# Kernel tuning notes

Hardware: AMD Instinct MI355X
Metric: run time of the kernel (lower is better)

Reference implementation:

```python
import jax, jax.numpy as jnp
import numpy as np

GROUPS = 32
EPS = 1e-5   # nn.GroupNorm default


def group_norm(x, gamma, beta):
    # x: [B, C, H, W]
    b, c, h, w = x.shape
    xg = x.reshape(b, GROUPS, c // GROUPS, h, w)
    mu = jnp.mean(xg, axis=(2, 3, 4), keepdims=True)
    var = jnp.var(xg, axis=(2, 3, 4), keepdims=True)
    xn = ((xg - mu) * jax.lax.rsqrt(var + EPS)).reshape(b, c, h, w)
    return xn * gamma[None, :, None, None] + beta[None, :, None, None]


def conv1x1(x, w, b):
    # x: [B, C, H, W], w: [O, C], b: [O]
    return jnp.einsum('bchw,oc->bohw', x, w) + b[None, :, None, None]


def setup_inputs() -> dict:
    key = jax.random.key(0)
    ks = jax.random.split(key, 10)
    B, C, H, W = 8, 512, 64, 64
    std = 1.0 / np.sqrt(C)
    inp = {
        'x': jax.random.normal(ks[0], (B, C, H, W), dtype=jnp.float32),
        'gn_gamma': jnp.ones((C,), dtype=jnp.float32),
        'gn_beta': jnp.zeros((C,), dtype=jnp.float32),
        'wq': jax.random.normal(ks[1], (C, C), dtype=jnp.float32) * std,
        'bq': jnp.zeros((C,), dtype=jnp.float32),
        'wk': jax.random.normal(ks[2], (C, C), dtype=jnp.float32) * std,
        'bk': jnp.zeros((C,), dtype=jnp.float32),
        'wv': jax.random.normal(ks[3], (C, C), dtype=jnp.float32) * std,
        'bv': jnp.zeros((C,), dtype=jnp.float32),
        'wp': jax.random.normal(ks[4], (C, C), dtype=jnp.float32) * std,
        'bp': jnp.zeros((C,), dtype=jnp.float32),
    }
    return inp


def reference(x, gn_gamma, gn_beta, wq, bq, wk, bk, wv, bv, wp, bp):
    b, c, hh, ww = x.shape
    n = hh * ww
    h = group_norm(x, gn_gamma, gn_beta)
    q = conv1x1(h, wq, bq).reshape(b, c, n).transpose(0, 2, 1)  # [B, N, C]
    k = conv1x1(h, wk, bk).reshape(b, c, n)                     # [B, C, N]
    v = conv1x1(h, wv, bv).reshape(b, c, n).transpose(0, 2, 1)  # [B, N, C]
    scale = 1.0 / jnp.sqrt(jnp.asarray(c, dtype=x.dtype))
    attn = jax.nn.softmax(jnp.einsum('bnc,bcm->bnm', q, k) * scale, axis=-1)
    out = jnp.einsum('bnm,bmc->bnc', attn, v)                   # [B, N, C]
    out = out.transpose(0, 2, 1).reshape(b, c, hh, ww)
    return x + conv1x1(out, wp, bp)
```

## Files before the change

kernel.cpp:

```cpp
#include <hip/hip_runtime.h>


typedef __attribute__((ext_vector_type(8))) __bf16 bf16x8;
typedef __attribute__((ext_vector_type(4))) float f32x4;
typedef unsigned int u32;

#define DEVICE __device__ __forceinline__

DEVICE void async_copy16(const void* g, void* l) {
  __builtin_amdgcn_global_load_lds(
      (__attribute__((address_space(1))) u32*)(g),
      (__attribute__((address_space(3))) u32*)(l),
      16, 0, 0);
}

__global__ __launch_bounds__(256) void cvt_w(
    const float* __restrict__ w0, const float* __restrict__ w1,
    const float* __restrict__ w2, const float* __restrict__ w3,
    __bf16* __restrict__ o0, __bf16* __restrict__ o1,
    __bf16* __restrict__ o2, __bf16* __restrict__ o3) {
  int idx = blockIdx.x * 256 + threadIdx.x;
  int off = idx * 8;
  int m = off >> 18;
  int r = off & 262143;
  const float* src = m == 0 ? w0 : m == 1 ? w1 : m == 2 ? w2 : w3;
  __bf16* dst = m == 0 ? o0 : m == 1 ? o1 : m == 2 ? o2 : o3;
  float4 a = *(const float4*)(src + r);
  float4 b = *(const float4*)(src + r + 4);
  bf16x8 v = {(__bf16)a.x, (__bf16)a.y, (__bf16)a.z, (__bf16)a.w,
              (__bf16)b.x, (__bf16)b.y, (__bf16)b.z, (__bf16)b.w};
  *(bf16x8*)(dst + r) = v;
}

__global__ __launch_bounds__(256) void gn_stats(const float* __restrict__ x,
                                                float* __restrict__ stats4) {
  int bg = blockIdx.x, qn = blockIdx.y;
  int t = threadIdx.x, lane = t & 63, w = t >> 6;
  float s = 0.f, ss = 0.f;
  for (int it = 0; it < 16; ++it) {
    int idx = it * 256 + t;
    int ch = idx >> 8, f4 = idx & 255;
    float4 v = *(const float4*)(x + (size_t)bg * 65536 + (size_t)ch * 4096 +
                                qn * 1024 + f4 * 4);
    s += v.x + v.y + v.z + v.w;
    ss += v.x * v.x + v.y * v.y + v.z * v.z + v.w * v.w;
  }
#pragma unroll
  for (int off = 32; off; off >>= 1) {
    s += __shfl_xor(s, off);
    ss += __shfl_xor(ss, off);
  }
  __shared__ float rs_[4], rss_[4];
  if (lane == 0) { rs_[w] = s; rss_[w] = ss; }
  __syncthreads();
  if (t == 0) {
    stats4[(bg * 4 + qn) * 2] = rs_[0] + rs_[1] + rs_[2] + rs_[3];
    stats4[(bg * 4 + qn) * 2 + 1] = rss_[0] + rss_[1] + rss_[2] + rss_[3];
  }
}

__global__ __launch_bounds__(256) void gn_apply(
    const float* __restrict__ x, const float* __restrict__ gamma,
    const float* __restrict__ beta, const float* __restrict__ stats4,
    __bf16* __restrict__ h) {
  int b = blockIdx.z, g4 = blockIdx.y;
  int n = blockIdx.x * 256 + threadIdx.x;
  float mean[4], rstd[4];
#pragma unroll
  for (int k = 0; k < 4; ++k) {
    int bg = b * 32 + g4 * 4 + k;
    float s = 0.f, ss = 0.f;
#pragma unroll
    for (int q = 0; q < 4; ++q) {
      s += stats4[(bg * 4 + q) * 2];
      ss += stats4[(bg * 4 + q) * 2 + 1];
    }
    float m = s * (1.0f / 65536.0f);
    mean[k] = m;
    rstd[k] = rsqrtf(ss * (1.0f / 65536.0f) - m * m + 1e-5f);
  }
  const float* px = x + ((size_t)b * 512 + g4 * 64) * 4096 + n;
  __bf16* dst = h + ((size_t)b * 4096 + n) * 512 + g4 * 64;
#pragma unroll
  for (int j4 = 0; j4 < 8; ++j4) {
    bf16x8 o;
#pragma unroll
    for (int e = 0; e < 8; ++e) {
      int c = j4 * 8 + e;
      int g = c >> 4;
      float v = px[(size_t)c * 4096];
      o[e] = (__bf16)((v - mean[g]) * rstd[g] * gamma[g4 * 64 + c] +
                      beta[g4 * 64 + c]);
    }
    *(bf16x8*)(dst + j4 * 8) = o;
  }
}


#define G256_PHASE(BUF, QR, QC, RDA, RDB, STAGE_STMT, TAIL_STMT)               \
  do {                                                                         \
    if (RDA) {                                                                 \
      _Pragma("unroll") for (int fr = 0; fr < 4; ++fr) {                       \
        a[fr][0] = ldA(BUF, (QR)*4 + fr, 0);                                   \
        a[fr][1] = ldA(BUF, (QR)*4 + fr, 1);                                   \
      }                                                                        \
    }                                                                          \
    if (RDB) {                                                                 \
      _Pragma("unroll") for (int fc = 0; fc < 2; ++fc) {                       \
        b[(QC)*2 + fc][0] = ldB(BUF, (QC)*2 + fc, 0);                          \
        b[(QC)*2 + fc][1] = ldB(BUF, (QC)*2 + fc, 1);                          \
      }                                                                        \
    }                                                                          \
    STAGE_STMT;                                                                \
    __builtin_amdgcn_s_barrier();                                              \
    asm volatile("s_waitcnt lgkmcnt(0)" ::: "memory");                         \
    __builtin_amdgcn_sched_barrier(0);                                         \
    __builtin_amdgcn_s_setprio(1);                                             \
    _Pragma("unroll") for (int fr = 0; fr < 4; ++fr)                           \
      _Pragma("unroll") for (int fc = 0; fc < 2; ++fc) {                       \
        acc[(QR)*4 + fr][(QC)*2 + fc] =                                        \
            __builtin_amdgcn_mfma_f32_16x16x32_bf16(                           \
                a[fr][0], b[(QC)*2 + fc][0], acc[(QR)*4 + fr][(QC)*2 + fc],    \
                0, 0, 0);                                                      \
        acc[(QR)*4 + fr][(QC)*2 + fc] =                                        \
            __builtin_amdgcn_mfma_f32_16x16x32_bf16(                           \
                a[fr][1], b[(QC)*2 + fc][1], acc[(QR)*4 + fr][(QC)*2 + fc],    \
                0, 0, 0);                                                      \
      }                                                                        \
    __builtin_amdgcn_s_setprio(0);                                             \
    TAIL_STMT;                                                                 \
    __builtin_amdgcn_sched_barrier(0);                                         \
    __builtin_amdgcn_s_barrier();                                              \
  } while (0)

#define G256_ITER(T0, T1, LAST)                                                \
  G256_PHASE(0, 0, 0, 1, 1, stage(1, 0, 0, (T1)), ((void)0));                  \
  G256_PHASE(0, 0, 1, 0, 1, stage(1, 0, 1, (T1)), ((void)0));                  \
  G256_PHASE(0, 1, 0, 1, 0,                                                    \
             if (!(LAST)) stage(0, 1, 0, (T0) + 2), ((void)0));                \
  G256_PHASE(0, 1, 1, 0, 0,                                                    \
             if (!(LAST)) stage(0, 1, 1, (T0) + 2),                            \
             if (LAST) {                                                       \
               asm volatile("s_waitcnt vmcnt(0)" ::: "memory");                \
             } else {                                                          \
               asm volatile("s_waitcnt vmcnt(4)" ::: "memory");                \
             });                                                               \
  G256_PHASE(1, 0, 0, 1, 1,                                                    \
             if (!(LAST)) stage(0, 0, 0, (T0) + 2), ((void)0));                \
  G256_PHASE(1, 0, 1, 0, 1,                                                    \
             if (!(LAST)) stage(0, 0, 1, (T0) + 2), ((void)0));                \
  G256_PHASE(1, 1, 0, 1, 0,                                                    \
             if (!(LAST)) stage(1, 1, 0, (T1) + 2), ((void)0));                \
  G256_PHASE(1, 1, 1, 0, 0,                                                    \
             if (!(LAST)) stage(1, 1, 1, (T1) + 2),                            \
             if (!(LAST)) {                                                    \
               asm volatile("s_waitcnt vmcnt(4)" ::: "memory");                \
             })

template <int EPI>
__global__ __launch_bounds__(512, 2) void gemm256(
    const __bf16* __restrict__ A, const __bf16* __restrict__ B,
    void* __restrict__ CoutV, int lda, int ldb, int ldc, int nIter, int nTM,
    int nTN, int KS, long sA, long sKA, long sB, long sKB, long sC,
    const float* __restrict__ bias0, const float* __restrict__ bias1,
    const float* __restrict__ resid) {
  __shared__ __bf16 lds_raw[2][2][2][128][64];

  int nwg = gridDim.x, bid = blockIdx.x;
  int qq = nwg >> 3, rr = nwg & 7;
  int xcd = bid & 7, ii = bid >> 3;
  int swz = (xcd < rr ? xcd * (qq + 1) : rr * (qq + 1) + (xcd - rr) * qq) + ii;
  int tn = swz % nTN;
  int tm = (swz / nTN) % nTM;
  int zz = swz / (nTN * nTM);
  int z = zz / KS, ks = zz % KS;
  A += (size_t)z * sA + (size_t)ks * sKA;
  B += (size_t)z * sB + (size_t)ks * sKB;
  __bf16* Cout = (__bf16*)CoutV + (size_t)zz * sC;
  int row0 = tm * 256, col0 = tn * 256;

  int tid = threadIdx.x;
  int wid = tid >> 6, lane = tid & 63;
  int wr = wid >> 2, wc = wid & 3;
  int l15 = lane & 15, l4 = lane >> 4;

  auto stage = [&](int buf, int mat, int half, int kt) {
    const __bf16* src = mat ? B : A;
    int ld = mat ? ldb : lda;
    int rbase = (mat ? col0 : row0) + half * 128;
    char* ldsbase = (char*)lds_raw + (((buf * 2 + mat) * 2 + half) * 16384);
#pragma unroll
    for (int L = 0; L < 2; ++L) {
      int ci = L * 512 + tid;
      int r = ci >> 3, cslot = ci & 7;
      int csrc = cslot ^ (r & 7);
      async_copy16(src + (size_t)(rbase + r) * ld + kt * 64 + csrc * 8,
                   ldsbase + (L * 512 + wid * 64) * 16);
    }
  };
  auto ldA = [&](int buf, int fr, int kh) -> bf16x8 {
    int row = fr * 16 + l15;
    int g = kh * 4 + l4;
    char* base = (char*)lds_raw + (((buf * 2 + 0) * 2 + wr) * 16384);
    return *(const bf16x8*)(base + row * 128 + ((g ^ (row & 7)) * 16));
  };
  auto ldB = [&](int buf, int fc, int kh) -> bf16x8 {
    int row = (wc & 1) * 64 + fc * 16 + l15;
    int g = kh * 4 + l4;
    char* base = (char*)lds_raw + (((buf * 2 + 1) * 2 + (wc >> 1)) * 16384);
    return *(const bf16x8*)(base + row * 128 + ((g ^ (row & 7)) * 16));
  };

  f32x4 acc[8][4] = {};
  bf16x8 a[4][2], b[4][2];

  stage(0, 1, 0, 0);
  stage(0, 1, 1, 0);
  stage(0, 0, 0, 0);
  stage(0, 0, 1, 0);
  stage(1, 1, 0, 1);
  stage(1, 1, 1, 1);
  asm volatile("s_waitcnt vmcnt(4)" ::: "memory");
  __builtin_amdgcn_sched_barrier(0);
  __builtin_amdgcn_s_barrier();

  int it = 0;
  for (; it < nIter - 1; ++it) {
    G256_ITER(2 * it, 2 * it + 1, 0);
  }
  G256_ITER(2 * it, 2 * it + 1, 1);

  int rb = row0 + wr * 128, cb = col0 + wc * 64;
  if constexpr (EPI == 3) {
#pragma unroll
    for (int fc = 0; fc < 4; ++fc) {
      int col = cb + fc * 16 + l15;
      float bb = bias0[col];
#pragma unroll
      for (int fr = 0; fr < 8; ++fr) {
        int r0 = rb + fr * 16 + l4 * 4;
        size_t idx = ((size_t)(r0 >> 12) * 512 + col) * 4096 + (r0 & 4095);
        float4 rv = *(const float4*)(resid + idx);
        float4 ov = {acc[fr][fc][0] + bb + rv.x, acc[fr][fc][1] + bb + rv.y,
                     acc[fr][fc][2] + bb + rv.z, acc[fr][fc][3] + bb + rv.w};
        *(float4*)((float*)CoutV + idx) = ov;
      }
    }
  } else {
#pragma unroll
    for (int fr = 0; fr < 8; ++fr) {
#pragma unroll
      for (int rg = 0; rg < 4; ++rg) {
        int row = rb + fr * 16 + l4 * 4 + rg;
#pragma unroll
        for (int fc = 0; fc < 4; ++fc) {
          int col = cb + fc * 16 + l15;
          float v = acc[fr][fc][rg];
          if constexpr (EPI == 1) v += col < 512 ? bias0[col] : bias1[col - 512];
          if constexpr (EPI == 2) v += bias0[row];
          Cout[(size_t)row * ldc + col] = (__bf16)v;
        }
      }
    }
  }
}

__global__ __launch_bounds__(256) void softmax_rows_bf16(__bf16* __restrict__ S) {
  int row = blockIdx.x;
  __bf16* p = S + (size_t)row * 4096;
  int t = threadIdx.x, lane = t & 63, w = t >> 6;
  const float c1 = 0.04419417382415922f * 1.4426950408889634f;
  bf16x8 v0 = *(const bf16x8*)(p + t * 16);
  bf16x8 v1 = *(const bf16x8*)(p + t * 16 + 8);
  float f[16];
  float mx = -3.4e38f;
#pragma unroll
  for (int i = 0; i < 8; ++i) { f[i] = (float)v0[i]; mx = fmaxf(mx, f[i]); }
#pragma unroll
  for (int i = 0; i < 8; ++i) { f[8 + i] = (float)v1[i]; mx = fmaxf(mx, f[8 + i]); }
#pragma unroll
  for (int off = 32; off; off >>= 1) mx = fmaxf(mx, __shfl_xor(mx, off));
  __shared__ float rm[4], rsum[4];
  if (lane == 0) rm[w] = mx;
  __syncthreads();
  float m = fmaxf(fmaxf(rm[0], rm[1]), fmaxf(rm[2], rm[3]));
  float s = 0.f;
#pragma unroll
  for (int i = 0; i < 16; ++i) {
    f[i] = exp2f((f[i] - m) * c1);
    s += f[i];
  }
#pragma unroll
  for (int off = 32; off; off >>= 1) s += __shfl_xor(s, off);
  if (lane == 0) rsum[w] = s;
  __syncthreads();
  float inv = 1.0f / (rsum[0] + rsum[1] + rsum[2] + rsum[3]);
  bf16x8 o0, o1;
#pragma unroll
  for (int i = 0; i < 8; ++i) o0[i] = (__bf16)(f[i] * inv);
#pragma unroll
  for (int i = 0; i < 8; ++i) o1[i] = (__bf16)(f[8 + i] * inv);
  *(bf16x8*)(p + t * 16) = o0;
  *(bf16x8*)(p + t * 16 + 8) = o1;
}

__global__ __launch_bounds__(256) void reduce4(const __bf16* __restrict__ part,
                                               __bf16* __restrict__ out) {
  int z = blockIdx.y;
  size_t e = ((size_t)blockIdx.x * 256 + threadIdx.x) * 8;
  const __bf16* p = part + (size_t)z * 4 * 2097152 + e;
  bf16x8 v0 = *(const bf16x8*)(p);
  bf16x8 v1 = *(const bf16x8*)(p + 2097152);
  bf16x8 v2 = *(const bf16x8*)(p + 2 * 2097152);
  bf16x8 v3 = *(const bf16x8*)(p + 3 * 2097152);
  bf16x8 o;
#pragma unroll
  for (int j = 0; j < 8; ++j)
    o[j] = (__bf16)((float)v0[j] + (float)v1[j] + (float)v2[j] + (float)v3[j]);
  *(bf16x8*)(out + (size_t)z * 2097152 + e) = o;
}

extern "C" void kernel_launch(void* const* d_in, const int* in_sizes, int n_in,
                              void* d_out, int out_size, void* d_ws, size_t ws_size,
                              hipStream_t stream) {
  const float* x = (const float*)d_in[0];
  const float* gamma = (const float*)d_in[1];
  const float* beta = (const float*)d_in[2];
  const float* wq = (const float*)d_in[3];
  const float* bq = (const float*)d_in[4];
  const float* wk = (const float*)d_in[5];
  const float* bk = (const float*)d_in[6];
  const float* wv = (const float*)d_in[7];
  const float* bv = (const float*)d_in[8];
  const float* wp = (const float*)d_in[9];
  const float* bp = (const float*)d_in[10];

  char* p = (char*)d_ws;
  auto alloc = [&](size_t bytes) {
    char* r = p;
    p += (bytes + 255) & ~(size_t)255;
    return r;
  };
  float* stats4 = (float*)alloc(256 * 4 * 2 * 4);
  __bf16* wqkb = (__bf16*)alloc((size_t)1024 * 512 * 2);
  __bf16* wvb = (__bf16*)alloc(512 * 512 * 2);
  __bf16* wpb = (__bf16*)alloc(512 * 512 * 2);
  __bf16* ho = (__bf16*)alloc((size_t)8 * 4096 * 512 * 2);
  __bf16* qk = (__bf16*)alloc((size_t)8 * 4096 * 1024 * 2);
  __bf16* vt = (__bf16*)alloc((size_t)8 * 512 * 4096 * 2);

  const size_t SB = (size_t)4096 * 4096 * 2;
  const size_t PB = (size_t)4 * 4096 * 512 * 2;
  size_t used = (size_t)(p - (char*)d_ws);
  size_t freeb = (ws_size > used) ? ws_size - used : 0;
  int nb = (int)(freeb / (SB + PB));
  if (nb > 8) nb = 8;
  if (nb < 1) nb = 1;
  __bf16* s = (__bf16*)alloc(SB * nb);
  __bf16* pvp = (__bf16*)alloc(PB * nb);

  cvt_w<<<512, 256, 0, stream>>>(wq, wk, wv, wp, wqkb, wqkb + 262144, wvb, wpb);
  gn_stats<<<dim3(256, 4), 256, 0, stream>>>(x, stats4);
  gn_apply<<<dim3(16, 8, 8), 256, 0, stream>>>(x, gamma, beta, stats4, ho);

  gemm256<1><<<dim3(512), 512, 0, stream>>>(
      ho, wqkb, qk, 512, 512, 1024, 4, 128, 4, 1, 0, 0, 0, 0, 0, bq, bk, nullptr);
  gemm256<2><<<dim3(256), 512, 0, stream>>>(
      wvb, ho, vt, 512, 512, 4096, 4, 2, 16, 1, 0, 0, 2097152, 0, 2097152,
      bv, nullptr, nullptr);

  __bf16* o = ho;
  for (int b0 = 0; b0 < 8; b0 += nb) {
    int zb = (8 - b0 < nb) ? (8 - b0) : nb;
    gemm256<0><<<dim3(zb * 256), 512, 0, stream>>>(
        qk + (size_t)b0 * 4194304, qk + (size_t)b0 * 4194304 + 512, s, 1024,
        1024, 4096, 4, 16, 16, 1, 4194304, 0, 4194304, 0, 16777216,
        nullptr, nullptr, nullptr);
    softmax_rows_bf16<<<zb * 4096, 256, 0, stream>>>(s);
    gemm256<0><<<dim3(zb * 128), 512, 0, stream>>>(
        s, vt + (size_t)b0 * 2097152, pvp, 4096, 4096, 512, 8, 16, 2, 4,
        16777216, 1024, 2097152, 1024, 2097152, nullptr, nullptr, nullptr);
    reduce4<<<dim3(1024, zb), 256, 0, stream>>>(pvp, o + (size_t)b0 * 2097152);
  }
  gemm256<3><<<dim3(256), 512, 0, stream>>>(
      o, wpb, d_out, 512, 512, 0, 4, 128, 2, 1, 0, 0, 0, 0, 0, bp, nullptr, x);
}
```

Before: 601.8 us.

## Process multiple N-tiles per workgroup with continuous K pipeline across segments

Adds a segment mechanism to the 256x256 GEMM so a workgroup computes several consecutive column tiles, keeping the async LDS staging pipeline running across tile boundaries and writing out each tile's accumulators in between. The QK projection and the QK^T score GEMM now launch half as many workgroups, each doing two column segments. This aims to cut per-workgroup prologue and pipeline-drain cost and to reuse the A tile's neighbourhood in cache, at the cost of fewer workgroups (less parallelism and tail balance) and an epilogue stall in the middle of the pipeline.

Result: slower. 664.9 us (+10.5%).

```diff
diff --git a/kernel.cpp b/kernel.cpp
--- a/kernel.cpp
+++ b/kernel.cpp
@@ -161,9 +161,9 @@
 __global__ __launch_bounds__(512, 2) void gemm256(
     const __bf16* __restrict__ A, const __bf16* __restrict__ B,
     void* __restrict__ CoutV, int lda, int ldb, int ldc, int nIter, int nTM,
-    int nTN, int KS, long sA, long sKA, long sB, long sKB, long sC,
-    const float* __restrict__ bias0, const float* __restrict__ bias1,
-    const float* __restrict__ resid) {
+    int nTN, int KS, int nseg, int ktShift, long sA, long sKA, long sB,
+    long sKB, long sC, const float* __restrict__ bias0,
+    const float* __restrict__ bias1, const float* __restrict__ resid) {
   __shared__ __bf16 lds_raw[2][2][2][128][64];
 
   int nwg = gridDim.x, bid = blockIdx.x;
@@ -177,7 +177,8 @@
   A += (size_t)z * sA + (size_t)ks * sKA;
   B += (size_t)z * sB + (size_t)ks * sKB;
   __bf16* Cout = (__bf16*)CoutV + (size_t)zz * sC;
-  int row0 = tm * 256, col0 = tn * 256;
+  int row0 = tm * 256, col0 = tn * 256 * nseg;
+  int ktMask = (1 << ktShift) - 1;
 
   int tid = threadIdx.x;
   int wid = tid >> 6, lane = tid & 63;
@@ -185,16 +186,18 @@
   int l15 = lane & 15, l4 = lane >> 4;
 
   auto stage = [&](int buf, int mat, int half, int kt) {
+    int seg = kt >> ktShift;
+    int ktE = kt & ktMask;
     const __bf16* src = mat ? B : A;
     int ld = mat ? ldb : lda;
-    int rbase = (mat ? col0 : row0) + half * 128;
+    int rbase = (mat ? col0 + seg * 256 : row0) + half * 128;
     char* ldsbase = (char*)lds_raw + (((buf * 2 + mat) * 2 + half) * 16384);
 #pragma unroll
     for (int L = 0; L < 2; ++L) {
       int ci = L * 512 + tid;
       int r = ci >> 3, cslot = ci & 7;
       int csrc = cslot ^ (r & 7);
-      async_copy16(src + (size_t)(rbase + r) * ld + kt * 64 + csrc * 8,
+      async_copy16(src + (size_t)(rbase + r) * ld + ktE * 64 + csrc * 8,
                    ldsbase + (L * 512 + wid * 64) * 16);
     }
   };
@@ -214,6 +217,43 @@
   f32x4 acc[8][4] = {};
   bf16x8 a[4][2], b[4][2];
 
+  auto wr_out = [&](int seg) {
+    int rb = row0 + wr * 128, cb = col0 + seg * 256 + wc * 64;
+    if constexpr (EPI == 3) {
+#pragma unroll
+      for (int fc = 0; fc < 4; ++fc) {
+        int col = cb + fc * 16 + l15;
+        float bb = bias0[col];
+#pragma unroll
+        for (int fr = 0; fr < 8; ++fr) {
+          int r0 = rb + fr * 16 + l4 * 4;
+          size_t idx = ((size_t)(r0 >> 12) * 512 + col) * 4096 + (r0 & 4095);
+          float4 rv = *(const float4*)(resid + idx);
+          float4 ov = {acc[fr][fc][0] + bb + rv.x, acc[fr][fc][1] + bb + rv.y,
+                       acc[fr][fc][2] + bb + rv.z, acc[fr][fc][3] + bb + rv.w};
+          *(float4*)((float*)CoutV + idx) = ov;
+        }
+      }
+    } else {
+#pragma unroll
+      for (int fr = 0; fr < 8; ++fr) {
+#pragma unroll
+        for (int rg = 0; rg < 4; ++rg) {
+          int row = rb + fr * 16 + l4 * 4 + rg;
+#pragma unroll
+          for (int fc = 0; fc < 4; ++fc) {
+            int col = cb + fc * 16 + l15;
+            float v = acc[fr][fc][rg];
+            if constexpr (EPI == 1)
+              v += col < 512 ? bias0[col] : bias1[col - 512];
+            if constexpr (EPI == 2) v += bias0[row];
+            Cout[(size_t)row * ldc + col] = (__bf16)v;
+          }
+        }
+      }
+    }
+  };
+
   stage(0, 1, 0, 0);
   stage(0, 1, 1, 0);
   stage(0, 0, 0, 0);
@@ -224,45 +264,23 @@
   __builtin_amdgcn_sched_barrier(0);
   __builtin_amdgcn_s_barrier();
 
+  int segIters = nIter / nseg;
   int it = 0;
-  for (; it < nIter - 1; ++it) {
+  for (int seg = 0; seg < nseg - 1; ++seg) {
+    for (int k = 0; k < segIters; ++k, ++it) {
+      G256_ITER(2 * it, 2 * it + 1, 0);
+    }
+    wr_out(seg);
+#pragma unroll
+    for (int i = 0; i < 8; ++i)
+#pragma unroll
+      for (int j = 0; j < 4; ++j) acc[i][j] = (f32x4){0.f, 0.f, 0.f, 0.f};
+  }
+  for (int k = 0; k < segIters - 1; ++k, ++it) {
     G256_ITER(2 * it, 2 * it + 1, 0);
   }
   G256_ITER(2 * it, 2 * it + 1, 1);
-
-  int rb = row0 + wr * 128, cb = col0 + wc * 64;
-  if constexpr (EPI == 3) {
-#pragma unroll
-    for (int fc = 0; fc < 4; ++fc) {
-      int col = cb + fc * 16 + l15;
-      float bb = bias0[col];
-#pragma unroll
-      for (int fr = 0; fr < 8; ++fr) {
-        int r0 = rb + fr * 16 + l4 * 4;
-        size_t idx = ((size_t)(r0 >> 12) * 512 + col) * 4096 + (r0 & 4095);
-        float4 rv = *(const float4*)(resid + idx);
-        float4 ov = {acc[fr][fc][0] + bb + rv.x, acc[fr][fc][1] + bb + rv.y,
-                     acc[fr][fc][2] + bb + rv.z, acc[fr][fc][3] + bb + rv.w};
-        *(float4*)((float*)CoutV + idx) = ov;
-      }
-    }
-  } else {
-#pragma unroll
-    for (int fr = 0; fr < 8; ++fr) {
-#pragma unroll
-      for (int rg = 0; rg < 4; ++rg) {
-        int row = rb + fr * 16 + l4 * 4 + rg;
-#pragma unroll
-        for (int fc = 0; fc < 4; ++fc) {
-          int col = cb + fc * 16 + l15;
-          float v = acc[fr][fc][rg];
-          if constexpr (EPI == 1) v += col < 512 ? bias0[col] : bias1[col - 512];
-          if constexpr (EPI == 2) v += bias0[row];
-          Cout[(size_t)row * ldc + col] = (__bf16)v;
-        }
-      }
-    }
-  }
+  wr_out(nseg - 1);
 }
 
 __global__ __launch_bounds__(256) void softmax_rows_bf16(__bf16* __restrict__ S) {
@@ -363,25 +381,27 @@
   gn_stats<<<dim3(256, 4), 256, 0, stream>>>(x, stats4);
   gn_apply<<<dim3(16, 8, 8), 256, 0, stream>>>(x, gamma, beta, stats4, ho);
 
-  gemm256<1><<<dim3(512), 512, 0, stream>>>(
-      ho, wqkb, qk, 512, 512, 1024, 4, 128, 4, 1, 0, 0, 0, 0, 0, bq, bk, nullptr);
+  gemm256<1><<<dim3(256), 512, 0, stream>>>(
+      ho, wqkb, qk, 512, 512, 1024, 8, 128, 2, 1, 2, 3, 0, 0, 0, 0, 0,
+      bq, bk, nullptr);
   gemm256<2><<<dim3(256), 512, 0, stream>>>(
-      wvb, ho, vt, 512, 512, 4096, 4, 2, 16, 1, 0, 0, 2097152, 0, 2097152,
-      bv, nullptr, nullptr);
+      wvb, ho, vt, 512, 512, 4096, 4, 2, 16, 1, 1, 10, 0, 0, 2097152, 0,
+      2097152, bv, nullptr, nullptr);
 
   __bf16* o = ho;
   for (int b0 = 0; b0 < 8; b0 += nb) {
     int zb = (8 - b0 < nb) ? (8 - b0) : nb;
-    gemm256<0><<<dim3(zb * 256), 512, 0, stream>>>(
+    gemm256<0><<<dim3(zb * 128), 512, 0, stream>>>(
         qk + (size_t)b0 * 4194304, qk + (size_t)b0 * 4194304 + 512, s, 1024,
-        1024, 4096, 4, 16, 16, 1, 4194304, 0, 4194304, 0, 16777216,
+        1024, 4096, 8, 16, 8, 1, 2, 3, 4194304, 0, 4194304, 0, 16777216,
         nullptr, nullptr, nullptr);
     softmax_rows_bf16<<<zb * 4096, 256, 0, stream>>>(s);
     gemm256<0><<<dim3(zb * 128), 512, 0, stream>>>(
-        s, vt + (size_t)b0 * 2097152, pvp, 4096, 4096, 512, 8, 16, 2, 4,
+        s, vt + (size_t)b0 * 2097152, pvp, 4096, 4096, 512, 8, 16, 2, 4, 1, 10,
         16777216, 1024, 2097152, 1024, 2097152, nullptr, nullptr, nullptr);
     reduce4<<<dim3(1024, zb), 256, 0, stream>>>(pvp, o + (size_t)b0 * 2097152);
   }
   gemm256<3><<<dim3(256), 512, 0, stream>>>(
-      o, wpb, d_out, 512, 512, 0, 4, 128, 2, 1, 0, 0, 0, 0, 0, bp, nullptr, x);
-}
+      o, wpb, d_out, 512, 512, 0, 4, 128, 2, 1, 1, 10, 0, 0, 0, 0, 0,
+      bp, nullptr, x);
+}
```
